# Optimization experiments

Hardware: AMD Instinct MI355X
Metric: run time of the kernel (lower is better)

The kernel has to match this reference:

```python
import jax, jax.numpy as jnp
import numpy as np
from jax import lax

VOCAB, EMBED, HIDDEN, LAYERS = 32000, 256, 384, 6
B, S = 16, 512
SCALE = 0.05  # keep tanh out of saturation

def setup_inputs() -> dict:
    key = jax.random.key(0)
    ks = jax.random.split(key, 10)
    return {
        "x": jax.random.randint(ks[0], (B, S), 0, VOCAB),
        "emb": jax.random.normal(ks[1], (VOCAB, EMBED), jnp.float32) * SCALE,
        "W_ih0": jax.random.normal(ks[2], (HIDDEN, EMBED), jnp.float32) * SCALE,
        "W_ih": jax.random.normal(ks[3], (LAYERS - 1, HIDDEN, HIDDEN), jnp.float32) * SCALE,
        "W_hh": jax.random.normal(ks[4], (LAYERS, HIDDEN, HIDDEN), jnp.float32) * SCALE,
        "b_ih": jax.random.normal(ks[5], (LAYERS, HIDDEN), jnp.float32) * SCALE,
        "b_hh": jax.random.normal(ks[6], (LAYERS, HIDDEN), jnp.float32) * SCALE,
        "W_out": jax.random.normal(ks[7], (VOCAB, HIDDEN), jnp.float32) * SCALE,
        "b_out": jax.random.normal(ks[8], (VOCAB,), jnp.float32) * SCALE,
    }

def _rnn_layer(seq, Wi, Wh, bi, bh):
    # seq: [S, B, in_dim]; Elman: h_t = tanh(x_t Wi^T + bi + h_{t-1} Wh^T + bh)
    pre = jnp.einsum('sbi,hi->sbh', seq, Wi) + bi  # batched input projection
    h0 = jnp.zeros((seq.shape[1], Wh.shape[0]), seq.dtype)
    def step(h, p):
        h = jnp.tanh(p + h @ Wh.T + bh)
        return h, h
    _, out = lax.scan(step, h0, pre)
    return out  # [S, B, H]

def reference(x, emb, W_ih0, W_ih, W_hh, b_ih, b_hh, W_out, b_out):
    seq = jnp.swapaxes(emb[x], 0, 1)  # [S, B, E]
    for l in range(LAYERS):
        Wi = W_ih0 if l == 0 else W_ih[l - 1]
        seq = _rnn_layer(seq, Wi, W_hh[l], b_ih[l], b_hh[l])
        # inter-layer dropout: identity in eval mode
    out = jnp.swapaxes(seq, 0, 1)  # [B, S, H]
    return out @ W_out.T + b_out  # [B, S, V]
```

## Files before the change

### kernel.cpp

```cpp
#include <hip/hip_runtime.h>

typedef _Float16 f16;
typedef _Float16 f16x8 __attribute__((ext_vector_type(8)));
typedef _Float16 f16x4 __attribute__((ext_vector_type(4)));
typedef float f32x4 __attribute__((ext_vector_type(4)));

#define MFMA16(a, b, c) __builtin_amdgcn_mfma_f32_16x16x32_f16(a, b, c, 0, 0, 0)

#define CH 8
#define NCH 64
#define SLOT_F (CH * 24 * 64 * 4)

__device__ __forceinline__ float fast_tanh(float x) {
    float e = __builtin_amdgcn_exp2f(x * 2.885390081777927f);
    return 1.0f - 2.0f * __builtin_amdgcn_rcpf(e + 1.0f);
}

__device__ __forceinline__ void lds_barrier() {
    asm volatile("s_waitcnt lgkmcnt(0)" ::: "memory");
    __builtin_amdgcn_s_barrier();
    __builtin_amdgcn_sched_barrier(0);
}

__device__ __forceinline__ void wait_flag(const int* f, int target) {
    if (threadIdx.x == 0) {
        while (__hip_atomic_load(f, __ATOMIC_ACQUIRE, __HIP_MEMORY_SCOPE_AGENT) < target) {
            __builtin_amdgcn_s_sleep(1);
        }
    }
    __syncthreads();
}
__device__ __forceinline__ void set_flag(int* f, int val) {
    __syncthreads();
    if (threadIdx.x == 0)
        __hip_atomic_store(f, val, __ATOMIC_RELEASE, __HIP_MEMORY_SCOPE_AGENT);
}

__global__ void cvt_kernel(const float* __restrict__ src, f16* __restrict__ dst, const int n4) {
    const int i = blockIdx.x * blockDim.x + threadIdx.x;
    if (i < n4) {
        const float4 v = ((const float4*)src)[i];
        f16x4 o = { (f16)v.x, (f16)v.y, (f16)v.z, (f16)v.w };
        *(f16x4*)(dst + (size_t)i * 4) = o;
    }
}

__global__ void bias_combine_kernel(const float* __restrict__ b_ih, const float* __restrict__ b_hh,
                                    float* __restrict__ bias_c) {
    const int i = blockIdx.x * blockDim.x + threadIdx.x;
    if (i < 6 * 384) bias_c[i] = b_ih[i] + b_hh[i];
}

__global__ void embed_kernel(const int* __restrict__ x, const float* __restrict__ emb,
                             f16* __restrict__ seq0) {
    const int token = blockIdx.x;
    const int s = token >> 4, b = token & 15;
    const int idx = x[b * 512 + s];
    const float4 v = ((const float4*)(emb + (size_t)idx * 256))[threadIdx.x];
    f16x4 o = { (f16)v.x, (f16)v.y, (f16)v.z, (f16)v.w };
    *(f16x4*)(seq0 + (size_t)token * 256 + threadIdx.x * 4) = o;
}

template<int NK>
__device__ __forceinline__ void a_role(const f16* __restrict__ in_seq,
                                       const f16* __restrict__ Wi,
                                       const float* __restrict__ bias,
                                       float* __restrict__ preL,
                                       const int* flag_in, int* flag_pre, const int* flag_seq,
                                       const int L) {
    const int tid = threadIdx.x, lane = tid & 63, w = tid >> 6;
    const int lr = lane & 15, lq = lane >> 4;
    const int KIN = NK * 32;

    f16x8 WiF[6][NK];
#pragma unroll
    for (int i = 0; i < 6; ++i) {
        const f16* wrow = Wi + (size_t)((w * 6 + i) * 16 + lr) * KIN + lq * 8;
#pragma unroll
        for (int kk = 0; kk < NK; ++kk) WiF[i][kk] = *(const f16x8*)(wrow + kk * 32);
    }
    float bv[6];
#pragma unroll
    for (int i = 0; i < 6; ++i) bv[i] = bias[(w * 6 + i) * 16 + lr];

    for (int c = 0; c < NCH; ++c) {
        if (L > 0) wait_flag(flag_in, c + 1);
        if (c >= 4) wait_flag(flag_seq, c - 3);

        float* slot = preL + (size_t)(c & 3) * SLOT_F;
#pragma unroll
        for (int g = 0; g < 2; ++g) {
            f32x4 acc[4][6];
#pragma unroll
            for (int s = 0; s < 4; ++s)
#pragma unroll
                for (int i = 0; i < 6; ++i) acc[s][i] = (f32x4){ bv[i], bv[i], bv[i], bv[i] };

            const int t0 = c * CH + g * 4;
#pragma unroll
            for (int kk = 0; kk < NK; ++kk) {
                f16x8 a[4];
#pragma unroll
                for (int s = 0; s < 4; ++s)
                    a[s] = *(const f16x8*)(in_seq + (size_t)((t0 + s) * 16 + lr) * KIN + kk * 32 + lq * 8);
#pragma unroll
                for (int s = 0; s < 4; ++s)
#pragma unroll
                    for (int i = 0; i < 6; ++i) acc[s][i] = MFMA16(a[s], WiF[i][kk], acc[s][i]);
            }
#pragma unroll
            for (int s = 0; s < 4; ++s)
#pragma unroll
                for (int i = 0; i < 6; ++i)
                    *(f32x4*)(slot + ((size_t)((g * 4 + s) * 24 + w * 6 + i) * 64 + lane) * 4) = acc[s][i];
        }
        set_flag(flag_pre, c + 1);
    }
}

__device__ __forceinline__ void b_role(const float* __restrict__ preL,
                                       const f16* __restrict__ Wh,
                                       f16* __restrict__ out_seq,
                                       const int* flag_pre, int* flag_seq,
                                       f16 (*hbuf)[16][392]) {
    const int tid = threadIdx.x, lane = tid & 63, w = tid >> 6;
    const int lr = lane & 15, lq = lane >> 4, kb = lq * 8;

    for (int i = tid; i < 2 * 16 * 392; i += 256) (&hbuf[0][0][0])[i] = (f16)0.0f;

    f16x8 WhF[6][12];
#pragma unroll
    for (int i = 0; i < 6; ++i) {
        const f16* wrow = Wh + (size_t)((w * 6 + i) * 16 + lr) * 384 + kb;
#pragma unroll
        for (int kk = 0; kk < 12; ++kk) WhF[i][kk] = *(const f16x8*)(wrow + kk * 32);
    }
    __syncthreads();

    const int crow = tid >> 4;
    const int ccol = (tid & 15) * 8;

    for (int c = 0; c < NCH; ++c) {
        wait_flag(flag_pre, c + 1);
        const float* slot = preL + (size_t)(c & 3) * SLOT_F;

#pragma unroll
        for (int g = 0; g < 2; ++g) {
            f32x4 pre_[4][6];
#pragma unroll
            for (int s = 0; s < 4; ++s)
#pragma unroll
                for (int i = 0; i < 6; ++i)
                    pre_[s][i] = *(const f32x4*)(slot + ((size_t)((g * 4 + s) * 24 + w * 6 + i) * 64 + lane) * 4);

#pragma unroll
            for (int s4 = 0; s4 < 4; ++s4) {
                const int sc = g * 4 + s4;
                const int t = c * CH + sc;
                f32x4 acc[6];
#pragma unroll
                for (int i = 0; i < 6; ++i) acc[i] = (f32x4){ 0.f, 0.f, 0.f, 0.f };

                const f16* hb = &hbuf[sc & 1][0][0] + lr * 392 + kb;
#pragma unroll
                for (int kk = 0; kk < 12; ++kk) {
                    const f16x8 a = *(const f16x8*)(hb + kk * 32);
#pragma unroll
                    for (int i = 0; i < 6; ++i) acc[i] = MFMA16(a, WhF[i][kk], acc[i]);
                }

                f16* hn = &hbuf[(sc + 1) & 1][0][0];
#pragma unroll
                for (int i = 0; i < 6; ++i) {
                    const int n = (w * 6 + i) * 16 + lr;
#pragma unroll
                    for (int r = 0; r < 4; ++r) {
                        const float v = acc[i][r] + pre_[s4][i][r];
                        hn[(lq * 4 + r) * 392 + n] = (f16)fast_tanh(v);
                    }
                }
                lds_barrier();
                const f16* hs = &hbuf[(sc + 1) & 1][0][0] + crow * 392 + ccol;
                f16* og = out_seq + (size_t)(t * 16 + crow) * 384 + ccol;
#pragma unroll
                for (int p = 0; p < 3; ++p)
                    *(f16x8*)(og + p * 128) = *(const f16x8*)(hs + p * 128);
            }
        }
        set_flag(flag_seq, c + 1);
    }
}

__global__ __launch_bounds__(256, 1) void pipeline_kernel(
    const f16* __restrict__ seq0, const f16* __restrict__ Wi0,
    const f16* __restrict__ WiR, const f16* __restrict__ WhAll,
    const float* __restrict__ biasAll, f16* __restrict__ sA, f16* __restrict__ sB,
    float* __restrict__ preRing, int* __restrict__ flags) {
    __shared__ f16 hbuf[2][16][392];
    const int bid = blockIdx.x;
    if (bid < 6) {
        const int L = bid;
        const f16* in_seq = (L == 0) ? seq0 : ((L & 1) ? sA : sB);
        const f16* Wi = (L == 0) ? Wi0 : (WiR + (size_t)(L - 1) * 384 * 384);
        float* preL = preRing + (size_t)L * 4 * SLOT_F;
        if (L == 0)
            a_role<8>(in_seq, Wi, biasAll, preL, nullptr, flags + 8, flags + 0, 0);
        else
            a_role<12>(in_seq, Wi, biasAll + L * 384, preL, flags + (L - 1), flags + 8 + L, flags + L, L);
    } else {
        const int L = bid - 6;
        f16* outb = (L & 1) ? sB : sA;
        b_role(preRing + (size_t)L * 4 * SLOT_F, WhAll + (size_t)L * 384 * 384, outb,
               flags + 8 + L, flags + L, hbuf);
    }
}

__global__ __launch_bounds__(256) void out_proj_kernel(
    const f16* __restrict__ A, const f16* __restrict__ Bm,
    const float* __restrict__ bias, float* __restrict__ C) {
    __shared__ f16 As[128][40];
    __shared__ f16 Bs[128][40];
    const int tid = threadIdx.x, lane = tid & 63, w = tid >> 6;
    const int lr = lane & 15, lq = lane >> 4;
    const int bm = blockIdx.x, bn = blockIdx.y;
    const int wm = w >> 1, wn = w & 1;

    f32x4 acc[4][4];
#pragma unroll
    for (int i = 0; i < 4; ++i)
#pragma unroll
        for (int j = 0; j < 4; ++j) acc[i][j] = (f32x4){ 0.f, 0.f, 0.f, 0.f };

    const int sr = tid >> 1, sh = tid & 1;
    const f16* Ag = A + (size_t)(bm * 128 + sr) * 384 + sh * 16;
    const f16* Bg = Bm + (size_t)(bn * 128 + sr) * 384 + sh * 16;

    for (int kt = 0; kt < 12; ++kt) {
        const f16x8 a0 = *(const f16x8*)(Ag + kt * 32);
        const f16x8 a1 = *(const f16x8*)(Ag + kt * 32 + 8);
        const f16x8 b0 = *(const f16x8*)(Bg + kt * 32);
        const f16x8 b1 = *(const f16x8*)(Bg + kt * 32 + 8);
        *(f16x8*)(&As[sr][sh * 16]) = a0;
        *(f16x8*)(&As[sr][sh * 16 + 8]) = a1;
        *(f16x8*)(&Bs[sr][sh * 16]) = b0;
        *(f16x8*)(&Bs[sr][sh * 16 + 8]) = b1;
        __syncthreads();
        f16x8 af[4], bf[4];
#pragma unroll
        for (int mi = 0; mi < 4; ++mi) af[mi] = *(const f16x8*)(&As[wm * 64 + mi * 16 + lr][lq * 8]);
#pragma unroll
        for (int ni = 0; ni < 4; ++ni) bf[ni] = *(const f16x8*)(&Bs[wn * 64 + ni * 16 + lr][lq * 8]);
#pragma unroll
        for (int mi = 0; mi < 4; ++mi)
#pragma unroll
            for (int ni = 0; ni < 4; ++ni) acc[mi][ni] = MFMA16(af[mi], bf[ni], acc[mi][ni]);
        __syncthreads();
    }

    float bv[4];
#pragma unroll
    for (int ni = 0; ni < 4; ++ni) bv[ni] = bias[bn * 128 + wn * 64 + ni * 16 + lr];
#pragma unroll
    for (int mi = 0; mi < 4; ++mi) {
#pragma unroll
        for (int rr = 0; rr < 4; ++rr) {
            const int m = bm * 128 + wm * 64 + mi * 16 + lq * 4 + rr;
            const int s = m >> 4, b = m & 15;
            float* crow = C + (size_t)(b * 512 + s) * 32000;
#pragma unroll
            for (int ni = 0; ni < 4; ++ni) {
                const int n = bn * 128 + wn * 64 + ni * 16 + lr;
                crow[n] = acc[mi][ni][rr] + bv[ni];
            }
        }
    }
}

extern "C" void kernel_launch(void* const* d_in, const int* in_sizes, int n_in,
                              void* d_out, int out_size, void* d_ws, size_t ws_size,
                              hipStream_t stream) {
    const int* x = (const int*)d_in[0];
    const float* emb = (const float*)d_in[1];
    const float* W_ih0 = (const float*)d_in[2];
    const float* W_ih = (const float*)d_in[3];
    const float* W_hh = (const float*)d_in[4];
    const float* b_ih = (const float*)d_in[5];
    const float* b_hh = (const float*)d_in[6];
    const float* W_out = (const float*)d_in[7];
    const float* b_out = (const float*)d_in[8];
    float* out = (float*)d_out;

    char* ws = (char*)d_ws;
    f16* Wi0_h = (f16*)(ws + 0);
    f16* Wi_h = (f16*)(ws + 196608);
    f16* Wh_h = (f16*)(ws + 1671168);
    f16* Wout_h = (f16*)(ws + 3440640);
    float* bias_c = (float*)(ws + 28016640);
    f16* seq0 = (f16*)(ws + 28025856);
    f16* sA = (f16*)(ws + 32220160);
    f16* sB = (f16*)(ws + 38511616);
    float* preRing = (float*)(ws + 44803072);
    int* flags = (int*)(ws + 49521664);
    if (ws_size < 49521920u) return;

    hipMemsetAsync(flags, 0, 256, stream);
    cvt_kernel<<<96, 256, 0, stream>>>(W_ih0, Wi0_h, 24576);
    cvt_kernel<<<720, 256, 0, stream>>>(W_ih, Wi_h, 184320);
    cvt_kernel<<<864, 256, 0, stream>>>(W_hh, Wh_h, 221184);
    cvt_kernel<<<12000, 256, 0, stream>>>(W_out, Wout_h, 3072000);
    bias_combine_kernel<<<9, 256, 0, stream>>>(b_ih, b_hh, bias_c);
    embed_kernel<<<8192, 64, 0, stream>>>(x, emb, seq0);

    pipeline_kernel<<<12, 256, 0, stream>>>(seq0, Wi0_h, Wi_h, Wh_h, bias_c,
                                            sA, sB, preRing, flags);

    dim3 g(64, 250);
    out_proj_kernel<<<g, 256, 0, stream>>>(sB, Wout_h, b_out, out);
}
```

Measured before the change: 1.913 ms.

## Store pre-activations as fp16, enlarge chunks, use LLC loads, swizzle output grid

The ring of input projections between the A and B roles is now stored in fp16 instead of fp32, and chunks are doubled to 16 timesteps. Activation and pre-activation loads go through inline-asm global loads with sc0 sc1 cache bits and explicit vmcnt waits so MFMAs can start while later loads are still arriving. The flag polling is relaxed from acquire to relaxed ordering. The output-projection grid is linearised and swizzled to improve L2 reuse of W_out tiles. Together these aim to cut inter-block transfer volume and synchronisation latency on the serial recurrence, at the cost of extra fp16 rounding on pre-activations and weaker memory ordering on the flags.

```diff
diff --git a/kernel.cpp b/kernel.cpp
--- a/kernel.cpp
+++ b/kernel.cpp
@@ -7,9 +7,9 @@
 
 #define MFMA16(a, b, c) __builtin_amdgcn_mfma_f32_16x16x32_f16(a, b, c, 0, 0, 0)
 
-#define CH 8
-#define NCH 64
-#define SLOT_F (CH * 24 * 64 * 4)
+#define CH 16
+#define NCH 32
+#define SLOT_H (CH * 24 * 64 * 4)
 
 __device__ __forceinline__ float fast_tanh(float x) {
     float e = __builtin_amdgcn_exp2f(x * 2.885390081777927f);
@@ -22,9 +22,25 @@
     __builtin_amdgcn_sched_barrier(0);
 }
 
+__device__ __forceinline__ f16x8 ld_llc(const f16* p) {
+    f16x8 v;
+    asm volatile("global_load_dwordx4 %0, %1, off sc0 sc1" : "=v"(v) : "v"(p) : "memory");
+    return v;
+}
+__device__ __forceinline__ f16x4 ld_llc_f16x4(const f16* p) {
+    f16x4 v;
+    asm volatile("global_load_dwordx2 %0, %1, off sc0 sc1" : "=v"(v) : "v"(p) : "memory");
+    return v;
+}
+
+#define VWAIT4(N, x0, x1, x2, x3) \
+    asm volatile("s_waitcnt vmcnt(" #N ")" : "+v"(x0), "+v"(x1), "+v"(x2), "+v"(x3))
+#define VWAITH6(N, p0, p1, p2, p3, p4, p5) \
+    asm volatile("s_waitcnt vmcnt(" #N ")" : "+v"(p0), "+v"(p1), "+v"(p2), "+v"(p3), "+v"(p4), "+v"(p5))
+
 __device__ __forceinline__ void wait_flag(const int* f, int target) {
     if (threadIdx.x == 0) {
-        while (__hip_atomic_load(f, __ATOMIC_ACQUIRE, __HIP_MEMORY_SCOPE_AGENT) < target) {
+        while (__hip_atomic_load(f, __ATOMIC_RELAXED, __HIP_MEMORY_SCOPE_AGENT) < target) {
             __builtin_amdgcn_s_sleep(1);
         }
     }
@@ -65,7 +81,7 @@
 __device__ __forceinline__ void a_role(const f16* __restrict__ in_seq,
                                        const f16* __restrict__ Wi,
                                        const float* __restrict__ bias,
-                                       float* __restrict__ preL,
+                                       f16* __restrict__ preL,
                                        const int* flag_in, int* flag_pre, const int* flag_seq,
                                        const int L) {
     const int tid = threadIdx.x, lane = tid & 63, w = tid >> 6;
@@ -87,38 +103,57 @@
         if (L > 0) wait_flag(flag_in, c + 1);
         if (c >= 4) wait_flag(flag_seq, c - 3);
 
-        float* slot = preL + (size_t)(c & 3) * SLOT_F;
-#pragma unroll
-        for (int g = 0; g < 2; ++g) {
-            f32x4 acc[4][6];
-#pragma unroll
-            for (int s = 0; s < 4; ++s)
-#pragma unroll
-                for (int i = 0; i < 6; ++i) acc[s][i] = (f32x4){ bv[i], bv[i], bv[i], bv[i] };
-
-            const int t0 = c * CH + g * 4;
-#pragma unroll
-            for (int kk = 0; kk < NK; ++kk) {
-                f16x8 a[4];
-#pragma unroll
-                for (int s = 0; s < 4; ++s)
-                    a[s] = *(const f16x8*)(in_seq + (size_t)((t0 + s) * 16 + lr) * KIN + kk * 32 + lq * 8);
-#pragma unroll
-                for (int s = 0; s < 4; ++s)
-#pragma unroll
-                    for (int i = 0; i < 6; ++i) acc[s][i] = MFMA16(a[s], WiF[i][kk], acc[s][i]);
+        f16* slot = preL + (size_t)(c & 3) * SLOT_H;
+#pragma unroll 1
+        for (int sc = 0; sc < CH; ++sc) {
+            const int t = c * CH + sc;
+            f32x4 acc[6];
+#pragma unroll
+            for (int i = 0; i < 6; ++i) acc[i] = (f32x4){ bv[i], bv[i], bv[i], bv[i] };
+
+            const f16* ar = in_seq + (size_t)(t * 16 + lr) * KIN + lq * 8;
+            f16x8 a[NK];
+#pragma unroll
+            for (int kk = 0; kk < NK; ++kk) a[kk] = ld_llc(ar + kk * 32);
+            if constexpr (NK == 12) {
+                VWAIT4(8, a[0], a[1], a[2], a[3]);
+#pragma unroll
+                for (int kk = 0; kk < 4; ++kk)
+#pragma unroll
+                    for (int i = 0; i < 6; ++i) acc[i] = MFMA16(a[kk], WiF[i][kk], acc[i]);
+                VWAIT4(4, a[4], a[5], a[6], a[7]);
+#pragma unroll
+                for (int kk = 4; kk < 8; ++kk)
+#pragma unroll
+                    for (int i = 0; i < 6; ++i) acc[i] = MFMA16(a[kk], WiF[i][kk], acc[i]);
+                VWAIT4(0, a[8], a[9], a[10], a[11]);
+#pragma unroll
+                for (int kk = 8; kk < 12; ++kk)
+#pragma unroll
+                    for (int i = 0; i < 6; ++i) acc[i] = MFMA16(a[kk], WiF[i][kk], acc[i]);
+            } else {
+                VWAIT4(4, a[0], a[1], a[2], a[3]);
+#pragma unroll
+                for (int kk = 0; kk < 4; ++kk)
+#pragma unroll
+                    for (int i = 0; i < 6; ++i) acc[i] = MFMA16(a[kk], WiF[i][kk], acc[i]);
+                VWAIT4(0, a[4], a[5], a[6], a[7]);
+#pragma unroll
+                for (int kk = 4; kk < 8; ++kk)
+#pragma unroll
+                    for (int i = 0; i < 6; ++i) acc[i] = MFMA16(a[kk], WiF[i][kk], acc[i]);
             }
 #pragma unroll
-            for (int s = 0; s < 4; ++s)
-#pragma unroll
-                for (int i = 0; i < 6; ++i)
-                    *(f32x4*)(slot + ((size_t)((g * 4 + s) * 24 + w * 6 + i) * 64 + lane) * 4) = acc[s][i];
+            for (int i = 0; i < 6; ++i) {
+                f16x4 ph = { (f16)acc[i][0], (f16)acc[i][1], (f16)acc[i][2], (f16)acc[i][3] };
+                *(f16x4*)(slot + ((size_t)(sc * 24 + w * 6 + i) * 64 + lane) * 4) = ph;
+            }
         }
         set_flag(flag_pre, c + 1);
     }
 }
 
-__device__ __forceinline__ void b_role(const float* __restrict__ preL,
+__device__ __forceinline__ void b_role(const f16* __restrict__ preL,
                                        const f16* __restrict__ Wh,
                                        f16* __restrict__ out_seq,
                                        const int* flag_pre, int* flag_seq,
@@ -142,16 +177,20 @@
 
     for (int c = 0; c < NCH; ++c) {
         wait_flag(flag_pre, c + 1);
-        const float* slot = preL + (size_t)(c & 3) * SLOT_F;
-
-#pragma unroll
-        for (int g = 0; g < 2; ++g) {
-            f32x4 pre_[4][6];
+        const f16* slot = preL + (size_t)(c & 3) * SLOT_H;
+
+#pragma unroll 1
+        for (int g = 0; g < CH / 4; ++g) {
+            f16x4 pr[4][6];
 #pragma unroll
             for (int s = 0; s < 4; ++s)
 #pragma unroll
                 for (int i = 0; i < 6; ++i)
-                    pre_[s][i] = *(const f32x4*)(slot + ((size_t)((g * 4 + s) * 24 + w * 6 + i) * 64 + lane) * 4);
+                    pr[s][i] = ld_llc_f16x4(slot + ((size_t)((g * 4 + s) * 24 + w * 6 + i) * 64 + lane) * 4);
+            VWAITH6(0, pr[0][0], pr[0][1], pr[0][2], pr[0][3], pr[0][4], pr[0][5]);
+            VWAITH6(0, pr[1][0], pr[1][1], pr[1][2], pr[1][3], pr[1][4], pr[1][5]);
+            VWAITH6(0, pr[2][0], pr[2][1], pr[2][2], pr[2][3], pr[2][4], pr[2][5]);
+            VWAITH6(0, pr[3][0], pr[3][1], pr[3][2], pr[3][3], pr[3][4], pr[3][5]);
 
 #pragma unroll
             for (int s4 = 0; s4 < 4; ++s4) {
@@ -175,7 +214,7 @@
                     const int n = (w * 6 + i) * 16 + lr;
 #pragma unroll
                     for (int r = 0; r < 4; ++r) {
-                        const float v = acc[i][r] + pre_[s4][i][r];
+                        const float v = acc[i][r] + (float)pr[s4][i][r];
                         hn[(lq * 4 + r) * 392 + n] = (f16)fast_tanh(v);
                     }
                 }
@@ -195,14 +234,14 @@
     const f16* __restrict__ seq0, const f16* __restrict__ Wi0,
     const f16* __restrict__ WiR, const f16* __restrict__ WhAll,
     const float* __restrict__ biasAll, f16* __restrict__ sA, f16* __restrict__ sB,
-    float* __restrict__ preRing, int* __restrict__ flags) {
+    f16* __restrict__ preRing, int* __restrict__ flags) {
     __shared__ f16 hbuf[2][16][392];
     const int bid = blockIdx.x;
     if (bid < 6) {
         const int L = bid;
         const f16* in_seq = (L == 0) ? seq0 : ((L & 1) ? sA : sB);
         const f16* Wi = (L == 0) ? Wi0 : (WiR + (size_t)(L - 1) * 384 * 384);
-        float* preL = preRing + (size_t)L * 4 * SLOT_F;
+        f16* preL = preRing + (size_t)L * 4 * SLOT_H;
         if (L == 0)
             a_role<8>(in_seq, Wi, biasAll, preL, nullptr, flags + 8, flags + 0, 0);
         else
@@ -210,7 +249,7 @@
     } else {
         const int L = bid - 6;
         f16* outb = (L & 1) ? sB : sA;
-        b_role(preRing + (size_t)L * 4 * SLOT_F, WhAll + (size_t)L * 384 * 384, outb,
+        b_role(preRing + (size_t)L * 4 * SLOT_H, WhAll + (size_t)L * 384 * 384, outb,
                flags + 8 + L, flags + L, hbuf);
     }
 }
@@ -222,7 +261,10 @@
     __shared__ f16 Bs[128][40];
     const int tid = threadIdx.x, lane = tid & 63, w = tid >> 6;
     const int lr = lane & 15, lq = lane >> 4;
-    const int bm = blockIdx.x, bn = blockIdx.y;
+    const int lin = blockIdx.x;
+    const int swz = (lin & 7) * 2000 + (lin >> 3);
+    const int bn = swz >> 6;
+    const int bm = swz & 63;
     const int wm = w >> 1, wn = w & 1;
 
     f32x4 acc[4][4];
@@ -299,7 +341,7 @@
     f16* seq0 = (f16*)(ws + 28025856);
     f16* sA = (f16*)(ws + 32220160);
     f16* sB = (f16*)(ws + 38511616);
-    float* preRing = (float*)(ws + 44803072);
+    f16* preRing = (f16*)(ws + 44803072);
     int* flags = (int*)(ws + 49521664);
     if (ws_size < 49521920u) return;
 
@@ -314,6 +356,5 @@
     pipeline_kernel<<<12, 256, 0, stream>>>(seq0, Wi0_h, Wi_h, Wh_h, bias_c,
                                             sA, sB, preRing, flags);
 
-    dim3 g(64, 250);
-    out_proj_kernel<<<g, 256, 0, stream>>>(sB, Wout_h, b_out, out);
-}
+    out_proj_kernel<<<16000, 256, 0, stream>>>(sB, Wout_h, b_out, out);
+}
```

Result: faster. 1.806 ms (-5.6%).
